# Kernel optimization log

Measured on AMD Instinct MI355X. Metric: run time of the kernel, lower is better.

Reference implementation:

```python
import jax, jax.numpy as jnp
import numpy as np

B, S, E, H = 2, 2048, 1024, 16
D = E // H  # head_dim = 64


def setup_inputs() -> dict:
    key = jax.random.key(0)
    ks = jax.random.split(key, 5)
    return {
        "hidden_states": jax.random.normal(ks[0], (B, S, E), jnp.float32),
        "c_attn_w": jax.random.normal(ks[1], (E, 3 * E), jnp.float32) * 0.02,
        "c_attn_b": jax.random.normal(ks[2], (3 * E,), jnp.float32) * 0.02,
        "c_proj_w": jax.random.normal(ks[3], (E, E), jnp.float32) * 0.02,
        "c_proj_b": jax.random.normal(ks[4], (E,), jnp.float32) * 0.02,
    }


def reference(hidden_states, c_attn_w, c_attn_b, c_proj_w, c_proj_b):
    # Conv1D: y = x @ W + b, W is [in, out]
    qkv = hidden_states @ c_attn_w + c_attn_b            # [B,S,3E]
    q, k, v = jnp.split(qkv, 3, axis=-1)                 # each [B,S,E]

    def split_heads(t):
        return t.reshape(B, S, H, D).transpose(0, 2, 1, 3)  # [B,H,S,D]

    q, k, v = split_heads(q), split_heads(k), split_heads(v)

    # scores scaled by 1/sqrt(head_dim) (scale_attn_weights=True)
    scores = jnp.einsum("bhqd,bhkd->bhqk", q, k) / jnp.asarray(
        np.sqrt(D), dtype=q.dtype
    )
    # causal mask: torch.where(causal, scores, finfo.min)
    causal = jnp.tril(jnp.ones((S, S), dtype=bool))
    mask_value = jnp.finfo(scores.dtype).min
    scores = jnp.where(causal[None, None], scores, mask_value)

    attn = jax.nn.softmax(scores, axis=-1)               # [B,H,S,S]
    out = jnp.einsum("bhqk,bhkd->bhqd", attn, v)          # [B,H,S,D]
    out = out.transpose(0, 2, 1, 3).reshape(B, S, E)      # merge heads
    out = out @ c_proj_w + c_proj_b                       # c_proj
    return out
```

## Files before the change

kernel.cpp:

```cpp
#include <hip/hip_runtime.h>
#include <stdint.h>

#define LOG2E 1.4426950408889634f
#define QSCALE (0.125f * LOG2E)

using u16 = unsigned short;
using u32 = unsigned int;

typedef __attribute__((ext_vector_type(8))) short short8;
typedef __attribute__((ext_vector_type(4))) float f32x4;
typedef __attribute__((ext_vector_type(16))) float f32x16;

__device__ __forceinline__ u16 f32_bf16(float f) {
  union { float f; u32 u; } v; v.f = f;
  u32 u = v.u;
  u += 0x7FFF + ((u >> 16) & 1);
  return (u16)(u >> 16);
}

__device__ __forceinline__ float max3f(float a, float b, float c) {
  return fmaxf(fmaxf(a, b), c);
}

__device__ __forceinline__ void gload_lds16(const void* g, void* l) {
  __builtin_amdgcn_global_load_lds(
      (const __attribute__((address_space(1))) u32*)(uintptr_t)g,
      (__attribute__((address_space(3))) u32*)(u32)(uintptr_t)l, 16, 0, 0);
}


__global__ __launch_bounds__(256) void cvt_f32_bf16(const float* __restrict__ in,
                                                    u16* __restrict__ out, int n4) {
  for (int i = blockIdx.x * blockDim.x + threadIdx.x; i < n4;
       i += gridDim.x * blockDim.x) {
    float4 v = ((const float4*)in)[i];
    union { u16 h[4]; uint2 u; } o;
    o.h[0] = f32_bf16(v.x); o.h[1] = f32_bf16(v.y);
    o.h[2] = f32_bf16(v.z); o.h[3] = f32_bf16(v.w);
    ((uint2*)out)[i] = o.u;
  }
}

__global__ __launch_bounds__(256) void transpose_bf16(const float* __restrict__ in,
                                                      u16* __restrict__ out,
                                                      int K, int N) {
  __shared__ float t[32][33];
  const int n0 = blockIdx.x * 32, k0 = blockIdx.y * 32;
  const int tx = threadIdx.x, ty = threadIdx.y;
#pragma unroll
  for (int j = 0; j < 32; j += 8)
    t[ty + j][tx] = in[(size_t)(k0 + ty + j) * N + n0 + tx];
  __syncthreads();
#pragma unroll
  for (int j = 0; j < 32; j += 8)
    out[(size_t)(n0 + ty + j) * K + k0 + tx] = f32_bf16(t[tx][ty + j]);
}

template <int MODE>
__global__ __launch_bounds__(256) void gemm_db(
    const u16* __restrict__ A, const u16* __restrict__ Bt,
    const float* __restrict__ bias,
    u16* __restrict__ qb, u16* __restrict__ kb, u16* __restrict__ vtb,
    float* __restrict__ fout) {
  __shared__ u16 lA[2][4096];
  __shared__ u16 lB[2][4096];
  const int tid = threadIdx.x;
  const int w = tid >> 6, l = tid & 63;
  const int l15 = l & 15, l4 = l >> 4;
  const int wr = w >> 1, wc = w & 1;
  const int bm = blockIdx.y, bn = blockIdx.x;
  const size_t m0 = (size_t)bm * 128, n0 = (size_t)bn * 128;

  f32x4 acc[4][4] = {};

  const int c = w * 64 + l;
  const int pair0 = c >> 3, s80 = c & 7;
  const int us8 = s80 ^ (pair0 & 7);
  const int grow = 2 * pair0 + (us8 >> 2);
  const int kslot = us8 & 3;
  const u16* gA = A + (m0 + grow) * 1024 + kslot * 8;
  const u16* gB = Bt + (n0 + grow) * 1024 + kslot * 8;

  auto stage = [&](int buf, int t) {
    const int k0 = t * 32;
    gload_lds16(gA + k0, lA[buf] + w * 512);
    gload_lds16(gA + k0 + 64 * 1024, lA[buf] + 2048 + w * 512);
    gload_lds16(gB + k0, lB[buf] + w * 512);
    gload_lds16(gB + k0 + 64 * 1024, lB[buf] + 2048 + w * 512);
  };

  stage(0, 0);
  stage(1, 1);

  for (int t = 0; t < 32; ++t) {
    const int buf = t & 1;
    if (t == 31) asm volatile("s_waitcnt vmcnt(0)" ::: "memory");
    else         asm volatile("s_waitcnt vmcnt(4)" ::: "memory");
    __builtin_amdgcn_s_barrier();
    __builtin_amdgcn_sched_barrier(0);
    short8 af[4], bf[4];
#pragma unroll
    for (int mI = 0; mI < 4; ++mI) {
      const int row = wr * 64 + mI * 16 + l15;
      const int pr = row >> 1;
      const int s8 = (((row & 1) << 2) | l4) ^ (pr & 7);
      af[mI] = *(const short8*)((const char*)lA[buf] + pr * 128 + s8 * 16);
    }
#pragma unroll
    for (int n = 0; n < 4; ++n) {
      const int row = wc * 64 + n * 16 + l15;
      const int pr = row >> 1;
      const int s8 = (((row & 1) << 2) | l4) ^ (pr & 7);
      bf[n] = *(const short8*)((const char*)lB[buf] + pr * 128 + s8 * 16);
    }
    __builtin_amdgcn_s_setprio(1);
#pragma unroll
    for (int mI = 0; mI < 4; ++mI)
#pragma unroll
      for (int n = 0; n < 4; ++n)
        acc[mI][n] = __builtin_amdgcn_mfma_f32_16x16x32_bf16(af[mI], bf[n], acc[mI][n], 0, 0, 0);
    __builtin_amdgcn_s_setprio(0);
    __builtin_amdgcn_s_barrier();
    if (t + 2 < 32) stage(buf, t + 2);
  }

  if (MODE == 0) {
#pragma unroll
    for (int mI = 0; mI < 4; ++mI) {
      const int row = (int)m0 + wr * 64 + mI * 16 + (l4 << 2);
      const int b = row >> 11, s = row & 2047;
#pragma unroll
      for (int n = 0; n < 4; ++n) {
        const int col = (int)n0 + wc * 64 + n * 16 + l15;
        const int part = col >> 10;
        const int h = (col & 1023) >> 6, d = col & 63;
        const float bv = bias[col];
        const size_t bh = (size_t)(b * 16 + h);
#pragma unroll
        for (int r = 0; r < 4; ++r) {
          const float v = acc[mI][n][r] + bv;
          const int ss = s + r;
          if (part == 0)
            qb[(bh * 2048 + ss) * 64 + d] = f32_bf16(v * QSCALE);
          else if (part == 1)
            kb[(bh * 2048 + ss) * 64 + d] = f32_bf16(v);
          else
            vtb[(bh * 64 + d) * 2048 + ss] = f32_bf16(v);
        }
      }
    }
  } else {
#pragma unroll
    for (int mI = 0; mI < 4; ++mI) {
      const size_t row = m0 + wr * 64 + mI * 16 + (l4 << 2);
#pragma unroll
      for (int n = 0; n < 4; ++n) {
        const size_t col = n0 + wc * 64 + n * 16 + l15;
        const float bv = bias[col];
#pragma unroll
        for (int r = 0; r < 4; ++r)
          fout[(row + r) * 1024 + col] = acc[mI][n][r] + bv;
      }
    }
  }
}

__global__ __launch_bounds__(256) void attn_fwd9(const u16* __restrict__ Qb,
                                                 const u16* __restrict__ Kb,
                                                 const u16* __restrict__ Vt,
                                                 u16* __restrict__ AO) {
  __shared__ u16 lK[2][4096];
  __shared__ u16 lV[2][4096];
  const int tid = threadIdx.x;
  const int l = tid & 63, w = tid >> 6;
  const int lq = l & 31, hi = l >> 5;
  const int bid = blockIdx.x;
  const int xcd = bid & 7, idx = bid >> 3;
  const int bh = xcd * 4 + (idx & 3);
  const int qb = 15 - (idx >> 2);
  const int qw = qb * 128 + w * 32;
  const int q = qw + lq;
  const int cdiag = 2 * qb + (w >> 1);
  const int NT = 2 * qb + 2;

  const u16* Qh = Qb + (size_t)bh * 131072;
  const u16* Kh = Kb + (size_t)bh * 131072;
  const u16* Vh = Vt + (size_t)bh * 131072;

  short8 qf[4];
#pragma unroll
  for (int kk = 0; kk < 4; ++kk)
    qf[kk] = *(const short8*)&Qh[(size_t)q * 64 + kk * 16 + hi * 8];

  f32x16 oA = {}, oB = {};
  float m = -3.0e38f, lsum = 0.f;

  const int srow = l >> 3, sslot = l & 7;
  const int swz = ((sslot ^ srow) << 3);
  const u16* kbase = Kh + (16 * w + srow) * 64 + swz;
  const u16* vbase = Vh + (size_t)(16 * w + srow) * 2048 + swz;
  char* lKw0 = (char*)&lK[0][0] + 2 * w * 1024;
  char* lVw0 = (char*)&lV[0][0] + 2 * w * 1024;

  auto stage = [&](int buf, int c) {
    const u16* ks = kbase + c * 4096;
    const u16* vs = vbase + c * 64;
    char* kd = lKw0 + buf * 8192;
    char* vd = lVw0 + buf * 8192;
    gload_lds16(ks, kd);
    gload_lds16(ks + 512, kd + 1024);
    gload_lds16(vs, vd);
    gload_lds16(vs + 16384, vd + 1024);
  };

  const int swsl = (lq & 7);

  auto pack16 = [&](const f32x16& st, short8& lo, short8& hi8) {
    u32 pk[8];
#pragma unroll
    for (int t2 = 0; t2 < 8; ++t2)
      asm("v_cvt_pk_bf16_f32 %0, %1, %2" : "=v"(pk[t2]) : "v"(st[2 * t2]), "v"(st[2 * t2 + 1]));
    u32 a0 = pk[0], a1 = pk[2]; asm("v_permlane32_swap_b32 %0, %1" : "+v"(a0), "+v"(a1));
    u32 a2 = pk[1], a3 = pk[3]; asm("v_permlane32_swap_b32 %0, %1" : "+v"(a2), "+v"(a3));
    u32 c0 = pk[4], c1 = pk[6]; asm("v_permlane32_swap_b32 %0, %1" : "+v"(c0), "+v"(c1));
    u32 c2 = pk[5], c3 = pk[7]; asm("v_permlane32_swap_b32 %0, %1" : "+v"(c2), "+v"(c3));
    union { u32 u[4]; short8 s; } f0, f1;
    f0.u[0] = a0; f0.u[1] = a2; f0.u[2] = a1; f0.u[3] = a3;
    f1.u[0] = c0; f1.u[1] = c2; f1.u[2] = c1; f1.u[3] = c3;
    lo = f0.s; hi8 = f1.s;
  };

  auto body64 = [&](int buf, bool mask2) {
    const char* kb = (const char*)&lK[buf][0] + lq * 128;
    const char* vb = (const char*)&lV[buf][0] + lq * 128;
    short8 kf0[4], kf1[4];
#pragma unroll
    for (int kk = 0; kk < 4; ++kk) {
      const int sl = ((2 * kk + hi) ^ swsl) << 4;
      kf0[kk] = *(const short8*)(kb + sl);
      kf1[kk] = *(const short8*)(kb + 4096 + sl);
    }
    f32x16 st0 = {}, st1 = {};
    __builtin_amdgcn_s_setprio(1);
#pragma unroll
    for (int kk = 0; kk < 4; ++kk)
      st0 = __builtin_amdgcn_mfma_f32_32x32x16_bf16(kf0[kk], qf[kk], st0, 0, 0, 0);
#pragma unroll
    for (int kk = 0; kk < 4; ++kk)
      st1 = __builtin_amdgcn_mfma_f32_32x32x16_bf16(kf1[kk], qf[kk], st1, 0, 0, 0);
    __builtin_amdgcn_s_setprio(0);

    short8 vfA[4], vfB[4];
#pragma unroll
    for (int ks = 0; ks < 4; ++ks) {
      const int sl = ((2 * ks + hi) ^ swsl) << 4;
      vfA[ks] = *(const short8*)(vb + sl);
      vfB[ks] = *(const short8*)(vb + 4096 + sl);
    }

    if (mask2) {
      const int qm = lq - hi * 4;
#pragma unroll
      for (int r = 0; r < 16; ++r) {
        const int t = (r & 3) + 8 * (r >> 2);
        if (t > qm) st1[r] = -3.0e38f;
      }
    }

    float a0 = max3f(st0[0], st0[1], st0[2]);
    float a1 = max3f(st0[3], st0[4], st0[5]);
    float a2 = max3f(st0[6], st0[7], st0[8]);
    float a3 = max3f(st0[9], st0[10], st0[11]);
    float a4 = max3f(st0[12], st0[13], st0[14]);
    float a5 = max3f(st0[15], st1[0], st1[1]);
    float a6 = max3f(st1[2], st1[3], st1[4]);
    float a7 = max3f(st1[5], st1[6], st1[7]);
    float a8 = max3f(st1[8], st1[9], st1[10]);
    float a9 = max3f(st1[11], st1[12], st1[13]);
    float a10 = fmaxf(st1[14], st1[15]);
    float b0 = max3f(a0, a1, a2);
    float b1 = max3f(a3, a4, a5);
    float b2 = max3f(a6, a7, a8);
    float b3 = max3f(a9, a10, b0);
    float pm = max3f(b1, b2, b3);
    pm = fmaxf(pm, __shfl_xor(pm, 32));

    if (!__all(pm <= m + 8.0f)) {
      const float mn = fmaxf(m, pm);
      const float alpha = __builtin_amdgcn_exp2f(m - mn);
      lsum *= alpha;
#pragma unroll
      for (int r = 0; r < 16; ++r) { oA[r] *= alpha; oB[r] *= alpha; }
      m = mn;
    }

#pragma unroll
    for (int r = 0; r < 16; ++r) st0[r] = __builtin_amdgcn_exp2f(st0[r] - m);
#pragma unroll
    for (int r = 0; r < 16; ++r) st1[r] = __builtin_amdgcn_exp2f(st1[r] - m);

    float s0 = (st0[0] + st0[1]) + (st0[2] + st0[3]);
    float s1 = (st0[4] + st0[5]) + (st0[6] + st0[7]);
    float s2 = (st0[8] + st0[9]) + (st0[10] + st0[11]);
    float s3 = (st0[12] + st0[13]) + (st0[14] + st0[15]);
    float s4 = (st1[0] + st1[1]) + (st1[2] + st1[3]);
    float s5 = (st1[4] + st1[5]) + (st1[6] + st1[7]);
    float s6 = (st1[8] + st1[9]) + (st1[10] + st1[11]);
    float s7 = (st1[12] + st1[13]) + (st1[14] + st1[15]);
    float rs = ((s0 + s1) + (s2 + s3)) + ((s4 + s5) + (s6 + s7));
    rs += __shfl_xor(rs, 32);
    lsum += rs;

    short8 pf0, pf1, pf2, pf3;
    pack16(st0, pf0, pf1);
    pack16(st1, pf2, pf3);

    __builtin_amdgcn_s_setprio(1);
    oA = __builtin_amdgcn_mfma_f32_32x32x16_bf16(vfA[0], pf0, oA, 0, 0, 0);
    oA = __builtin_amdgcn_mfma_f32_32x32x16_bf16(vfA[1], pf1, oA, 0, 0, 0);
    oA = __builtin_amdgcn_mfma_f32_32x32x16_bf16(vfA[2], pf2, oA, 0, 0, 0);
    oA = __builtin_amdgcn_mfma_f32_32x32x16_bf16(vfA[3], pf3, oA, 0, 0, 0);
    oB = __builtin_amdgcn_mfma_f32_32x32x16_bf16(vfB[0], pf0, oB, 0, 0, 0);
    oB = __builtin_amdgcn_mfma_f32_32x32x16_bf16(vfB[1], pf1, oB, 0, 0, 0);
    oB = __builtin_amdgcn_mfma_f32_32x32x16_bf16(vfB[2], pf2, oB, 0, 0, 0);
    oB = __builtin_amdgcn_mfma_f32_32x32x16_bf16(vfB[3], pf3, oB, 0, 0, 0);
    __builtin_amdgcn_s_setprio(0);
  };

  auto body32m = [&](int buf) {
    const char* kb = (const char*)&lK[buf][0] + lq * 128;
    const char* vb = (const char*)&lV[buf][0] + lq * 128;
    short8 kf0[4];
#pragma unroll
    for (int kk = 0; kk < 4; ++kk)
      kf0[kk] = *(const short8*)(kb + (((2 * kk + hi) ^ swsl) << 4));
    f32x16 st0 = {};
    __builtin_amdgcn_s_setprio(1);
#pragma unroll
    for (int kk = 0; kk < 4; ++kk)
      st0 = __builtin_amdgcn_mfma_f32_32x32x16_bf16(kf0[kk], qf[kk], st0, 0, 0, 0);
    __builtin_amdgcn_s_setprio(0);

    short8 vfA[2], vfB[2];
#pragma unroll
    for (int ks = 0; ks < 2; ++ks) {
      const int sl = ((2 * ks + hi) ^ swsl) << 4;
      vfA[ks] = *(const short8*)(vb + sl);
      vfB[ks] = *(const short8*)(vb + 4096 + sl);
    }

    const int qm = lq - hi * 4;
#pragma unroll
    for (int r = 0; r < 16; ++r) {
      const int t = (r & 3) + 8 * (r >> 2);
      if (t > qm) st0[r] = -3.0e38f;
    }
    float a0 = max3f(st0[0], st0[1], st0[2]);
    float a1 = max3f(st0[3], st0[4], st0[5]);
    float a2 = max3f(st0[6], st0[7], st0[8]);
    float a3 = max3f(st0[9], st0[10], st0[11]);
    float a4 = max3f(st0[12], st0[13], st0[14]);
    float b0 = max3f(a0, a1, a2);
    float b1 = max3f(a3, a4, st0[15]);
    float pm = fmaxf(b0, b1);
    pm = fmaxf(pm, __shfl_xor(pm, 32));
    if (!__all(pm <= m + 8.0f)) {
      const float mn = fmaxf(m, pm);
      const float alpha = __builtin_amdgcn_exp2f(m - mn);
      lsum *= alpha;
#pragma unroll
      for (int r = 0; r < 16; ++r) { oA[r] *= alpha; oB[r] *= alpha; }
      m = mn;
    }
#pragma unroll
    for (int r = 0; r < 16; ++r) st0[r] = __builtin_amdgcn_exp2f(st0[r] - m);
    float s0 = (st0[0] + st0[1]) + (st0[2] + st0[3]);
    float s1 = (st0[4] + st0[5]) + (st0[6] + st0[7]);
    float s2 = (st0[8] + st0[9]) + (st0[10] + st0[11]);
    float s3 = (st0[12] + st0[13]) + (st0[14] + st0[15]);
    float rs = (s0 + s1) + (s2 + s3);
    rs += __shfl_xor(rs, 32);
    lsum += rs;

    short8 pf0, pf1;
    pack16(st0, pf0, pf1);
    __builtin_amdgcn_s_setprio(1);
    oA = __builtin_amdgcn_mfma_f32_32x32x16_bf16(vfA[0], pf0, oA, 0, 0, 0);
    oA = __builtin_amdgcn_mfma_f32_32x32x16_bf16(vfA[1], pf1, oA, 0, 0, 0);
    oB = __builtin_amdgcn_mfma_f32_32x32x16_bf16(vfB[0], pf0, oB, 0, 0, 0);
    oB = __builtin_amdgcn_mfma_f32_32x32x16_bf16(vfB[1], pf1, oB, 0, 0, 0);
    __builtin_amdgcn_s_setprio(0);
  };

  stage(0, 0);
  stage(1, 1);
  for (int c = 0; c < NT; ++c) {
    const int buf = c & 1;
    if (c + 1 < NT) asm volatile("s_waitcnt vmcnt(4)" ::: "memory");
    else            asm volatile("s_waitcnt vmcnt(0)" ::: "memory");
    __builtin_amdgcn_s_barrier();
    __builtin_amdgcn_sched_barrier(0);
    if (c < cdiag) body64(buf, false);
    else if (c == cdiag) { if (w & 1) body64(buf, true); else body32m(buf); }
    __builtin_amdgcn_s_barrier();
    if (c + 2 < NT) stage(buf, c + 2);
  }

  const float rl = __builtin_amdgcn_rcpf(lsum);
  const int b = bh >> 4, h = bh & 15;
  u16* orow = AO + ((size_t)(b * 2048 + q)) * 1024 + h * 64;
#pragma unroll
  for (int g = 0; g < 4; ++g) {
    float e0 = oA[4 * g] * rl, e1 = oA[4 * g + 1] * rl;
    float e2 = oA[4 * g + 2] * rl, e3 = oA[4 * g + 3] * rl;
    float f0 = oB[4 * g] * rl, f1 = oB[4 * g + 1] * rl;
    float f2 = oB[4 * g + 2] * rl, f3 = oB[4 * g + 3] * rl;
    u32 w0, w1, w2, w3;
    asm("v_cvt_pk_bf16_f32 %0, %1, %2" : "=v"(w0) : "v"(e0), "v"(e1));
    asm("v_cvt_pk_bf16_f32 %0, %1, %2" : "=v"(w1) : "v"(e2), "v"(e3));
    asm("v_cvt_pk_bf16_f32 %0, %1, %2" : "=v"(w2) : "v"(f0), "v"(f1));
    asm("v_cvt_pk_bf16_f32 %0, %1, %2" : "=v"(w3) : "v"(f2), "v"(f3));
    uint2 uA; uA.x = w0; uA.y = w1;
    uint2 uB; uB.x = w2; uB.y = w3;
    *(uint2*)&orow[8 * g + 4 * hi] = uA;
    *(uint2*)&orow[32 + 8 * g + 4 * hi] = uB;
  }
}


extern "C" void kernel_launch(void* const* d_in, const int* in_sizes, int n_in,
                              void* d_out, int out_size, void* d_ws, size_t ws_size,
                              hipStream_t stream) {
  const float* hs = (const float*)d_in[0];
  const float* w1 = (const float*)d_in[1];
  const float* b1 = (const float*)d_in[2];
  const float* w2 = (const float*)d_in[3];
  const float* b2 = (const float*)d_in[4];
  float* out = (float*)d_out;

  char* ws = (char*)d_ws;
  u16* Xb  = (u16*)(ws);
  u16* W1t = (u16*)(ws + (8ull  << 20));
  u16* W2t = (u16*)(ws + (14ull << 20));
  u16* Qb  = (u16*)(ws + (16ull << 20));
  u16* Kb  = (u16*)(ws + (24ull << 20));
  u16* Vtb = (u16*)(ws + (32ull << 20));
  u16* AO  = (u16*)(ws + (40ull << 20));

  cvt_f32_bf16<<<dim3(2048), dim3(256), 0, stream>>>(hs, Xb, 4096 * 1024 / 4);
  transpose_bf16<<<dim3(96, 32), dim3(32, 8), 0, stream>>>(w1, W1t, 1024, 3072);
  transpose_bf16<<<dim3(32, 32), dim3(32, 8), 0, stream>>>(w2, W2t, 1024, 1024);
  gemm_db<0><<<dim3(24, 32), dim3(256), 0, stream>>>(Xb, W1t, b1, Qb, Kb, Vtb, nullptr);
  attn_fwd9<<<dim3(512), dim3(256), 0, stream>>>(Qb, Kb, Vtb, AO);
  gemm_db<1><<<dim3(8, 32), dim3(256), 0, stream>>>(AO, W2t, b2, nullptr, nullptr, nullptr, out);
}
```

Measured before the change: 118.1 us.

## Split attention KV loop across two wave groups with LDS softmax merge

Doubles the attention block to 512 threads: two groups of four waves each process alternating KV chunks for the same 128 query rows, halving the serial loop length per wave. At the end, group 1 writes its partial output, max and sum to LDS, and group 0 merges them with a rescaled log-sum-exp combine before writing bf16 output. This adds parallelism within each block to shorten the long causal tiles. The cost is doubled LDS, a merge step through shared memory, and possibly lower occupancy per CU.

```diff
diff --git a/kernel.cpp b/kernel.cpp
--- a/kernel.cpp
+++ b/kernel.cpp
@@ -165,23 +165,23 @@
   }
 }
 
-__global__ __launch_bounds__(256) void attn_fwd9(const u16* __restrict__ Qb,
-                                                 const u16* __restrict__ Kb,
-                                                 const u16* __restrict__ Vt,
-                                                 u16* __restrict__ AO) {
-  __shared__ u16 lK[2][4096];
-  __shared__ u16 lV[2][4096];
+__global__ __launch_bounds__(512) void attn_fwd10(const u16* __restrict__ Qb,
+                                                  const u16* __restrict__ Kb,
+                                                  const u16* __restrict__ Vt,
+                                                  u16* __restrict__ AO) {
+  __shared__ u16 lK[2][2][4096];
+  __shared__ u16 lV[2][2][4096];
   const int tid = threadIdx.x;
   const int l = tid & 63, w = tid >> 6;
+  const int g = w >> 2, wl = w & 3;
   const int lq = l & 31, hi = l >> 5;
   const int bid = blockIdx.x;
   const int xcd = bid & 7, idx = bid >> 3;
   const int bh = xcd * 4 + (idx & 3);
   const int qb = 15 - (idx >> 2);
-  const int qw = qb * 128 + w * 32;
-  const int q = qw + lq;
-  const int cdiag = 2 * qb + (w >> 1);
-  const int NT = 2 * qb + 2;
+  const int q = qb * 128 + wl * 32 + lq;
+  const int cdiag = 2 * qb + (wl >> 1);
+  const int NC = qb + 1;
 
   const u16* Qh = Qb + (size_t)bh * 131072;
   const u16* Kh = Kb + (size_t)bh * 131072;
@@ -197,16 +197,16 @@
 
   const int srow = l >> 3, sslot = l & 7;
   const int swz = ((sslot ^ srow) << 3);
-  const u16* kbase = Kh + (16 * w + srow) * 64 + swz;
-  const u16* vbase = Vh + (size_t)(16 * w + srow) * 2048 + swz;
-  char* lKw0 = (char*)&lK[0][0] + 2 * w * 1024;
-  char* lVw0 = (char*)&lV[0][0] + 2 * w * 1024;
-
-  auto stage = [&](int buf, int c) {
-    const u16* ks = kbase + c * 4096;
-    const u16* vs = vbase + c * 64;
-    char* kd = lKw0 + buf * 8192;
-    char* vd = lVw0 + buf * 8192;
+  const u16* kbase = Kh + (16 * wl + srow) * 64 + swz;
+  const u16* vbase = Vh + (size_t)(16 * wl + srow) * 2048 + swz;
+  char* lKg = (char*)&lK[g][0][0] + 2 * wl * 1024;
+  char* lVg = (char*)&lV[g][0][0] + 2 * wl * 1024;
+
+  auto stage = [&](int buf, int cabs) {
+    const u16* ks = kbase + cabs * 4096;
+    const u16* vs = vbase + cabs * 64;
+    char* kd = lKg + buf * 8192;
+    char* vd = lVg + buf * 8192;
     gload_lds16(ks, kd);
     gload_lds16(ks + 512, kd + 1024);
     gload_lds16(vs, vd);
@@ -231,8 +231,8 @@
   };
 
   auto body64 = [&](int buf, bool mask2) {
-    const char* kb = (const char*)&lK[buf][0] + lq * 128;
-    const char* vb = (const char*)&lV[buf][0] + lq * 128;
+    const char* kb = (const char*)&lK[g][buf][0] + lq * 128;
+    const char* vb = (const char*)&lV[g][buf][0] + lq * 128;
     short8 kf0[4], kf1[4];
 #pragma unroll
     for (int kk = 0; kk < 4; ++kk) {
@@ -328,8 +328,8 @@
   };
 
   auto body32m = [&](int buf) {
-    const char* kb = (const char*)&lK[buf][0] + lq * 128;
-    const char* vb = (const char*)&lV[buf][0] + lq * 128;
+    const char* kb = (const char*)&lK[g][buf][0] + lq * 128;
+    const char* vb = (const char*)&lV[g][buf][0] + lq * 128;
     short8 kf0[4];
 #pragma unroll
     for (int kk = 0; kk < 4; ++kk)
@@ -392,38 +392,63 @@
     __builtin_amdgcn_s_setprio(0);
   };
 
-  stage(0, 0);
-  stage(1, 1);
-  for (int c = 0; c < NT; ++c) {
-    const int buf = c & 1;
-    if (c + 1 < NT) asm volatile("s_waitcnt vmcnt(4)" ::: "memory");
+  stage(0, g);
+  if (NC > 1) stage(1, 2 + g);
+  for (int i = 0; i < NC; ++i) {
+    const int cabs = 2 * i + g;
+    const int buf = i & 1;
+    if (i + 1 < NC) asm volatile("s_waitcnt vmcnt(4)" ::: "memory");
     else            asm volatile("s_waitcnt vmcnt(0)" ::: "memory");
     __builtin_amdgcn_s_barrier();
     __builtin_amdgcn_sched_barrier(0);
-    if (c < cdiag) body64(buf, false);
-    else if (c == cdiag) { if (w & 1) body64(buf, true); else body32m(buf); }
+    if (cabs < cdiag) body64(buf, false);
+    else if (cabs == cdiag) { if (wl & 1) body64(buf, true); else body32m(buf); }
     __builtin_amdgcn_s_barrier();
-    if (c + 2 < NT) stage(buf, c + 2);
-  }
-
-  const float rl = __builtin_amdgcn_rcpf(lsum);
-  const int b = bh >> 4, h = bh & 15;
-  u16* orow = AO + ((size_t)(b * 2048 + q)) * 1024 + h * 64;
-#pragma unroll
-  for (int g = 0; g < 4; ++g) {
-    float e0 = oA[4 * g] * rl, e1 = oA[4 * g + 1] * rl;
-    float e2 = oA[4 * g + 2] * rl, e3 = oA[4 * g + 3] * rl;
-    float f0 = oB[4 * g] * rl, f1 = oB[4 * g + 1] * rl;
-    float f2 = oB[4 * g + 2] * rl, f3 = oB[4 * g + 3] * rl;
-    u32 w0, w1, w2, w3;
-    asm("v_cvt_pk_bf16_f32 %0, %1, %2" : "=v"(w0) : "v"(e0), "v"(e1));
-    asm("v_cvt_pk_bf16_f32 %0, %1, %2" : "=v"(w1) : "v"(e2), "v"(e3));
-    asm("v_cvt_pk_bf16_f32 %0, %1, %2" : "=v"(w2) : "v"(f0), "v"(f1));
-    asm("v_cvt_pk_bf16_f32 %0, %1, %2" : "=v"(w3) : "v"(f2), "v"(f3));
-    uint2 uA; uA.x = w0; uA.y = w1;
-    uint2 uB; uB.x = w2; uB.y = w3;
-    *(uint2*)&orow[8 * g + 4 * hi] = uA;
-    *(uint2*)&orow[32 + 8 * g + 4 * hi] = uB;
+    if (i + 2 < NC) stage(buf, 2 * (i + 2) + g);
+  }
+
+  float* mergeO  = (float*)&lK[0][0][0];
+  float* mergeML = (float*)&lV[0][0][0];
+  if (g == 1) {
+#pragma unroll
+    for (int r = 0; r < 16; ++r) {
+      mergeO[r * 256 + wl * 64 + l] = oA[r];
+      mergeO[(16 + r) * 256 + wl * 64 + l] = oB[r];
+    }
+    mergeML[wl * 64 + l] = m;
+    mergeML[512 + wl * 64 + l] = lsum;
+  }
+  __syncthreads();
+  if (g == 0) {
+    const float m1 = mergeML[wl * 64 + l];
+    const float l1 = mergeML[512 + wl * 64 + l];
+    const float M = fmaxf(m, m1);
+    const float sc0 = __builtin_amdgcn_exp2f(m - M);
+    const float sc1 = __builtin_amdgcn_exp2f(m1 - M);
+    const float L = lsum * sc0 + l1 * sc1;
+    const float rl = __builtin_amdgcn_rcpf(L);
+    const float a0 = sc0 * rl, a1 = sc1 * rl;
+    const int b = bh >> 4, h = bh & 15;
+    u16* orow = AO + ((size_t)(b * 2048 + q)) * 1024 + h * 64;
+#pragma unroll
+    for (int g4 = 0; g4 < 4; ++g4) {
+      float e[4], f[4];
+#pragma unroll
+      for (int t = 0; t < 4; ++t) {
+        const int r = 4 * g4 + t;
+        e[t] = oA[r] * a0 + mergeO[r * 256 + wl * 64 + l] * a1;
+        f[t] = oB[r] * a0 + mergeO[(16 + r) * 256 + wl * 64 + l] * a1;
+      }
+      u32 w0, w1, w2, w3;
+      asm("v_cvt_pk_bf16_f32 %0, %1, %2" : "=v"(w0) : "v"(e[0]), "v"(e[1]));
+      asm("v_cvt_pk_bf16_f32 %0, %1, %2" : "=v"(w1) : "v"(e[2]), "v"(e[3]));
+      asm("v_cvt_pk_bf16_f32 %0, %1, %2" : "=v"(w2) : "v"(f[0]), "v"(f[1]));
+      asm("v_cvt_pk_bf16_f32 %0, %1, %2" : "=v"(w3) : "v"(f[2]), "v"(f[3]));
+      uint2 uA; uA.x = w0; uA.y = w1;
+      uint2 uB; uB.x = w2; uB.y = w3;
+      *(uint2*)&orow[8 * g4 + 4 * hi] = uA;
+      *(uint2*)&orow[32 + 8 * g4 + 4 * hi] = uB;
+    }
   }
 }
 
@@ -451,6 +476,6 @@
   transpose_bf16<<<dim3(96, 32), dim3(32, 8), 0, stream>>>(w1, W1t, 1024, 3072);
   transpose_bf16<<<dim3(32, 32), dim3(32, 8), 0, stream>>>(w2, W2t, 1024, 1024);
   gemm_db<0><<<dim3(24, 32), dim3(256), 0, stream>>>(Xb, W1t, b1, Qb, Kb, Vtb, nullptr);
-  attn_fwd9<<<dim3(512), dim3(256), 0, stream>>>(Qb, Kb, Vtb, AO);
+  attn_fwd10<<<dim3(512), dim3(512), 0, stream>>>(Qb, Kb, Vtb, AO);
   gemm_db<1><<<dim3(8, 32), dim3(256), 0, stream>>>(AO, W2t, b2, nullptr, nullptr, nullptr, out);
 }
```

Result: faster. 107.4 us (-9.1%).
